# Performance work log

Hardware: AMD Instinct MI355X
Metric: run time of the kernel (lower is better)

Reference implementation:

```python
import jax, jax.numpy as jnp
import numpy as np

NUM_CLASS = 50000
HIDDEN = 512


def setup_inputs() -> dict:
    key = jax.random.key(0)
    ks = jax.random.split(key, 16)
    H, V = HIDDEN, NUM_CLASS
    return {
        # forward args
        "inputX": jax.random.randint(ks[0], (1,), 0, V),
        "hourX": jax.random.randint(ks[1], (1,), 0, 24),
        "weekdayX": jax.random.randint(ks[2], (1,), 0, 7),
        "intervalX": jax.random.uniform(ks[3], (1,), dtype=jnp.float32),
        "h": jax.random.normal(ks[4], (1, H), dtype=jnp.float32),
        "h3": jax.random.normal(ks[5], (1, H), dtype=jnp.float32),
        # parameters (torch Linear convention: weight [out, in])
        "emb": jax.random.normal(ks[6], (V, H), dtype=jnp.float32) * 0.02,
        "W_h3": jax.random.normal(ks[7], (H, H), dtype=jnp.float32) * 0.05,
        "b_h3": jax.random.normal(ks[8], (H,), dtype=jnp.float32) * 0.05,
        "W_int": jax.random.normal(ks[9], (H, 1), dtype=jnp.float32) * 0.05,
        "b_int": jax.random.normal(ks[10], (H,), dtype=jnp.float32) * 0.05,
        "W_ctx": jax.random.normal(ks[11], (H * H, H), dtype=jnp.float32) * 0.02,
        "b_ctx": jax.random.normal(ks[12], (H * H,), dtype=jnp.float32) * 0.02,
        "b_ictx": jax.random.normal(ks[13], (H,), dtype=jnp.float32) * 0.05,
        "Wx": jax.random.normal(ks[14], (H, H), dtype=jnp.float32) * 0.05,
        "Bx": jax.random.normal(ks[15], (H,), dtype=jnp.float32) * 0.05,
        "fc_W": jax.random.normal(jax.random.fold_in(key, 100), (V, H), dtype=jnp.float32) * 0.02,
        "fc_b": jax.random.normal(jax.random.fold_in(key, 101), (V,), dtype=jnp.float32) * 0.02,
    }


def reference(inputX, hourX, weekdayX, intervalX, h, h3,
              emb, W_h3, b_h3, W_int, b_int, W_ctx, b_ctx, b_ictx,
              Wx, Bx, fc_W, fc_b):
    H = h.shape[-1]
    sig = jax.nn.sigmoid
    # embedding lookup: [1, H]
    x_emb = emb[inputX]
    # h3 update: F.linear(intervalX, W_int, b_int) + LinearH3(h3)
    # W_int: [H, 1] so the interval linear is intervalX * W_int[:, 0] + b_int
    h3_new = sig(intervalX[:, None] * W_int[:, 0][None, :] + b_int
                 + h3 @ W_h3.T + b_h3)                      # [1, H]
    # hypernetwork: per-step context weight matrix [H, H]
    ctx = sig(h3_new @ W_ctx.T + b_ctx).reshape(H, H)
    # gated recurrent update
    h_new = sig(x_emb @ Wx.T + Bx + h @ ctx.T + b_ictx)      # [1, H]
    logits = h_new @ fc_W.T + fc_b                           # [1, V]
    # original returns (logits, h, h2, h3); h2 is unused/None
    return logits, h_new, h3_new
```

## Files before the change

### kernel.cpp

```cpp
#include <hip/hip_runtime.h>

#define H 512
#define V 50000

typedef float fx4 __attribute__((ext_vector_type(4)));

__device__ __forceinline__ float sigmoidf(float x) {
    return 1.0f / (1.0f + __expf(-x));
}

__device__ __forceinline__ float wave_reduce(float v) {
    #pragma unroll
    for (int m = 32; m >= 1; m >>= 1)
        v += __shfl_xor(v, m, 64);
    return v;
}

__device__ __forceinline__ float dot4(fx4 a, fx4 b) {
    return a.x * b.x + a.y * b.y + a.z * b.z + a.w * b.w;
}

__device__ __forceinline__ fx4 ntload4(const float* p) {
    return __builtin_nontemporal_load((const fx4*)p);
}

__device__ __forceinline__ fx4 ld4(const float* p) {
    return *(const fx4*)p;
}

__global__ __launch_bounds__(128) void kA(
    const float* __restrict__ intervalX, const float* __restrict__ h3,
    const float* __restrict__ W_h3, const float* __restrict__ b_h3,
    const float* __restrict__ W_int, const float* __restrict__ b_int,
    float* __restrict__ out)
{
    const int tid  = threadIdx.x;
    const int wv   = tid >> 6;
    const int lane = tid & 63;
    const int r    = blockIdx.x * 2 + wv;

    const float* Wrow = W_h3 + (size_t)r * H;
    fx4 a0 = ld4(Wrow + lane * 4);
    fx4 a1 = ld4(Wrow + 256 + lane * 4);
    fx4 x0 = ld4(h3 + lane * 4);
    fx4 x1 = ld4(h3 + 256 + lane * 4);
    float p = dot4(a0, x0) + dot4(a1, x1);
    p = wave_reduce(p);

    if (lane == 0) {
        float pre = p + intervalX[0] * W_int[r] + b_int[r] + b_h3[r];
        out[V + H + r] = sigmoidf(pre);
    }
}

__global__ __launch_bounds__(1024) void kB(
    const int* __restrict__ inputX, const float* __restrict__ emb,
    const float* __restrict__ h, const float* __restrict__ W_ctx,
    const float* __restrict__ b_ctx, const float* __restrict__ h3n,
    const float* __restrict__ Wx, const float* __restrict__ Bx,
    const float* __restrict__ b_ictx, float* __restrict__ out)
{
    __shared__ float sh3[H];
    __shared__ float sh[H];
    __shared__ float semb[H];
    __shared__ float sbc[H];
    __shared__ float red[16];

    const int tid = threadIdx.x;
    const int j   = blockIdx.x;
    const size_t base = (size_t)j * H;

    const float* embrow = emb + (size_t)inputX[0] * H;
    if (tid < H) {
        sh3[tid]  = h3n[tid];
        semb[tid] = embrow[tid];
    } else {
        const int t = tid - H;
        sh[t]  = h[t];
        sbc[t] = b_ctx[base + t];
    }
    __syncthreads();

    const int wv   = tid >> 6;
    const int lane = tid & 63;

    const fx4 x0 = ld4(sh3 + lane * 4);
    const fx4 x1 = ld4(sh3 + 256 + lane * 4);

    float acc = 0.0f;

    if (wv == 0) {
        const float* Wxrow = Wx + (size_t)j * H;
        fx4 a0 = ld4(Wxrow + lane * 4);
        fx4 a1 = ld4(Wxrow + 256 + lane * 4);
        float p = dot4(a0, ld4(semb + lane * 4)) + dot4(a1, ld4(semb + 256 + lane * 4));
        p = wave_reduce(p);
        acc += p + Bx[j] + b_ictx[j];
    }

    if ((j & 3) == 0) {
        #pragma unroll 4
        for (int i = 0; i < 32; ++i) {
            const int k = wv * 32 + i;
            const float* Wrow = W_ctx + (base + (size_t)k) * H;
            fx4 a0 = ld4(Wrow + lane * 4);
            fx4 a1 = ld4(Wrow + 256 + lane * 4);
            float p = dot4(a0, x0) + dot4(a1, x1);
            p = wave_reduce(p);
            acc += sh[k] * sigmoidf(p + sbc[k]);
        }
    } else {
        #pragma unroll 4
        for (int i = 0; i < 32; ++i) {
            const int k = wv * 32 + i;
            const float* Wrow = W_ctx + (base + (size_t)k) * H;
            fx4 a0 = ntload4(Wrow + lane * 4);
            fx4 a1 = ntload4(Wrow + 256 + lane * 4);
            float p = dot4(a0, x0) + dot4(a1, x1);
            p = wave_reduce(p);
            acc += sh[k] * sigmoidf(p + sbc[k]);
        }
    }

    if (lane == 0) red[wv] = acc;
    __syncthreads();

    if (tid == 0) {
        float t = 0.0f;
        #pragma unroll
        for (int w = 0; w < 16; ++w) t += red[w];
        out[V + j] = sigmoidf(t);
    }
}

__global__ __launch_bounds__(256) void kC(
    const float* __restrict__ h_new, const float* __restrict__ fc_W,
    const float* __restrict__ fc_b, float* __restrict__ out)
{
    __shared__ float shn[H];
    const int tid = threadIdx.x;
    shn[tid]       = h_new[tid];
    shn[tid + 256] = h_new[tid + 256];
    __syncthreads();

    const int wv   = tid >> 6;
    const int lane = tid & 63;
    const fx4 x0 = ld4(shn + lane * 4);
    const fx4 x1 = ld4(shn + 256 + lane * 4);

    const int rbase = blockIdx.x * 16 + wv * 4;
    #pragma unroll
    for (int r = 0; r < 4; ++r) {
        const int v = rbase + r;
        const float* Wrow = fc_W + (size_t)v * H;
        fx4 a0 = ld4(Wrow + lane * 4);
        fx4 a1 = ld4(Wrow + 256 + lane * 4);
        float p = dot4(a0, x0) + dot4(a1, x1);
        p = wave_reduce(p);
        if (lane == 0) out[v] = p + fc_b[v];
    }
}

extern "C" void kernel_launch(void* const* d_in, const int* in_sizes, int n_in,
                              void* d_out, int out_size, void* d_ws, size_t ws_size,
                              hipStream_t stream) {
    const int*   inputX    = (const int*)d_in[0];
    const float* intervalX = (const float*)d_in[3];
    const float* h         = (const float*)d_in[4];
    const float* h3        = (const float*)d_in[5];
    const float* emb       = (const float*)d_in[6];
    const float* W_h3      = (const float*)d_in[7];
    const float* b_h3      = (const float*)d_in[8];
    const float* W_int     = (const float*)d_in[9];
    const float* b_int     = (const float*)d_in[10];
    const float* W_ctx     = (const float*)d_in[11];
    const float* b_ctx     = (const float*)d_in[12];
    const float* b_ictx    = (const float*)d_in[13];
    const float* Wx        = (const float*)d_in[14];
    const float* Bx        = (const float*)d_in[15];
    const float* fc_W      = (const float*)d_in[16];
    const float* fc_b      = (const float*)d_in[17];

    float* out = (float*)d_out;

    kA<<<256, 128, 0, stream>>>(intervalX, h3, W_h3, b_h3, W_int, b_int, out);
    kB<<<512, 1024, 0, stream>>>(inputX, emb, h, W_ctx, b_ctx, out + V + H,
                                 Wx, Bx, b_ictx, out);
    kC<<<3125, 256, 0, stream>>>(out + V, fc_W, fc_b, out);
}
```

Measured before the change: 108.5 us.

## Fuse three kernels into one persistent kernel with grid barrier

Merges the h3 update, hypernetwork context GEMV and final logits GEMV into a single 512-block kernel. Each block recomputes h3_new redundantly (256 KB of W_h3 reads per block, mostly served from cache), and an atomic counter acts as a grid-wide barrier before the fc_W phase. This removes two kernel launches and the gaps between them. In exchange it adds a memset, redundant compute, and a spin barrier that deadlocks unless all 512 blocks of 1024 threads are co-resident.

```diff
diff --git a/kernel.cpp b/kernel.cpp
--- a/kernel.cpp
+++ b/kernel.cpp
@@ -2,6 +2,8 @@
 
 #define H 512
 #define V 50000
+#define NBLK 512
+#define NTHR 1024
 
 typedef float fx4 __attribute__((ext_vector_type(4)));
 
@@ -28,73 +30,64 @@
     return *(const fx4*)p;
 }
 
-__global__ __launch_bounds__(128) void kA(
-    const float* __restrict__ intervalX, const float* __restrict__ h3,
+__global__ __launch_bounds__(NTHR, 8) void fused(
+    const int* __restrict__ inputX, const float* __restrict__ intervalX,
+    const float* __restrict__ h, const float* __restrict__ h3,
+    const float* __restrict__ emb,
     const float* __restrict__ W_h3, const float* __restrict__ b_h3,
     const float* __restrict__ W_int, const float* __restrict__ b_int,
-    float* __restrict__ out)
+    const float* __restrict__ W_ctx, const float* __restrict__ b_ctx,
+    const float* __restrict__ b_ictx,
+    const float* __restrict__ Wx, const float* __restrict__ Bx,
+    const float* __restrict__ fc_W, const float* __restrict__ fc_b,
+    float* __restrict__ out, int* __restrict__ cnt)
 {
+    __shared__ float sh3[H];
+    __shared__ float sh[H];
+    __shared__ float sbc[H];
+    __shared__ float red[16];
+
     const int tid  = threadIdx.x;
     const int wv   = tid >> 6;
     const int lane = tid & 63;
-    const int r    = blockIdx.x * 2 + wv;
-
-    const float* Wrow = W_h3 + (size_t)r * H;
-    fx4 a0 = ld4(Wrow + lane * 4);
-    fx4 a1 = ld4(Wrow + 256 + lane * 4);
-    fx4 x0 = ld4(h3 + lane * 4);
-    fx4 x1 = ld4(h3 + 256 + lane * 4);
-    float p = dot4(a0, x0) + dot4(a1, x1);
-    p = wave_reduce(p);
-
-    if (lane == 0) {
-        float pre = p + intervalX[0] * W_int[r] + b_int[r] + b_h3[r];
-        out[V + H + r] = sigmoidf(pre);
-    }
-}
-
-__global__ __launch_bounds__(1024) void kB(
-    const int* __restrict__ inputX, const float* __restrict__ emb,
-    const float* __restrict__ h, const float* __restrict__ W_ctx,
-    const float* __restrict__ b_ctx, const float* __restrict__ h3n,
-    const float* __restrict__ Wx, const float* __restrict__ Bx,
-    const float* __restrict__ b_ictx, float* __restrict__ out)
-{
-    __shared__ float sh3[H];
-    __shared__ float sh[H];
-    __shared__ float semb[H];
-    __shared__ float sbc[H];
-    __shared__ float red[16];
-
-    const int tid = threadIdx.x;
-    const int j   = blockIdx.x;
+    const int j    = blockIdx.x;
     const size_t base = (size_t)j * H;
 
-    const float* embrow = emb + (size_t)inputX[0] * H;
-    if (tid < H) {
-        sh3[tid]  = h3n[tid];
-        semb[tid] = embrow[tid];
-    } else {
-        const int t = tid - H;
-        sh[t]  = h[t];
-        sbc[t] = b_ctx[base + t];
+    if (tid < H) sh[tid] = h[tid];
+    else { const int t = tid - H; sbc[t] = b_ctx[base + t]; }
+
+    {
+        const float ivx = intervalX[0];
+        const fx4 x0 = ld4(h3 + lane * 4);
+        const fx4 x1 = ld4(h3 + 256 + lane * 4);
+        #pragma unroll 4
+        for (int i = 0; i < 32; ++i) {
+            const int k = wv * 32 + i;
+            const float* Wrow = W_h3 + (size_t)k * H;
+            fx4 a0 = ld4(Wrow + lane * 4);
+            fx4 a1 = ld4(Wrow + 256 + lane * 4);
+            float p = wave_reduce(dot4(a0, x0) + dot4(a1, x1));
+            if (lane == 0) {
+                float v = sigmoidf(p + ivx * W_int[k] + b_int[k] + b_h3[k]);
+                sh3[k] = v;
+                if (j == 0) out[V + H + k] = v;
+            }
+        }
     }
     __syncthreads();
-
-    const int wv   = tid >> 6;
-    const int lane = tid & 63;
 
     const fx4 x0 = ld4(sh3 + lane * 4);
     const fx4 x1 = ld4(sh3 + 256 + lane * 4);
 
     float acc = 0.0f;
-
     if (wv == 0) {
         const float* Wxrow = Wx + (size_t)j * H;
+        const float* e = emb + (size_t)inputX[0] * H;
         fx4 a0 = ld4(Wxrow + lane * 4);
         fx4 a1 = ld4(Wxrow + 256 + lane * 4);
-        float p = dot4(a0, ld4(semb + lane * 4)) + dot4(a1, ld4(semb + 256 + lane * 4));
-        p = wave_reduce(p);
+        fx4 e0 = ld4(e + lane * 4);
+        fx4 e1 = ld4(e + 256 + lane * 4);
+        float p = wave_reduce(dot4(a0, e0) + dot4(a1, e1));
         acc += p + Bx[j] + b_ictx[j];
     }
 
@@ -105,8 +98,7 @@
             const float* Wrow = W_ctx + (base + (size_t)k) * H;
             fx4 a0 = ld4(Wrow + lane * 4);
             fx4 a1 = ld4(Wrow + 256 + lane * 4);
-            float p = dot4(a0, x0) + dot4(a1, x1);
-            p = wave_reduce(p);
+            float p = wave_reduce(dot4(a0, x0) + dot4(a1, x1));
             acc += sh[k] * sigmoidf(p + sbc[k]);
         }
     } else {
@@ -116,8 +108,7 @@
             const float* Wrow = W_ctx + (base + (size_t)k) * H;
             fx4 a0 = ntload4(Wrow + lane * 4);
             fx4 a1 = ntload4(Wrow + 256 + lane * 4);
-            float p = dot4(a0, x0) + dot4(a1, x1);
-            p = wave_reduce(p);
+            float p = wave_reduce(dot4(a0, x0) + dot4(a1, x1));
             acc += sh[k] * sigmoidf(p + sbc[k]);
         }
     }
@@ -130,34 +121,31 @@
         #pragma unroll
         for (int w = 0; w < 16; ++w) t += red[w];
         out[V + j] = sigmoidf(t);
+        __threadfence();
+        __hip_atomic_fetch_add(cnt, 1, __ATOMIC_RELEASE, __HIP_MEMORY_SCOPE_AGENT);
+        while (__hip_atomic_load(cnt, __ATOMIC_RELAXED, __HIP_MEMORY_SCOPE_AGENT) < NBLK) {
+            __builtin_amdgcn_s_sleep(2);
+        }
     }
-}
+    __syncthreads();
+    __threadfence();
 
-__global__ __launch_bounds__(256) void kC(
-    const float* __restrict__ h_new, const float* __restrict__ fc_W,
-    const float* __restrict__ fc_b, float* __restrict__ out)
-{
-    __shared__ float shn[H];
-    const int tid = threadIdx.x;
-    shn[tid]       = h_new[tid];
-    shn[tid + 256] = h_new[tid + 256];
+    if (tid < H) sh3[tid] = out[V + tid];
     __syncthreads();
 
-    const int wv   = tid >> 6;
-    const int lane = tid & 63;
-    const fx4 x0 = ld4(shn + lane * 4);
-    const fx4 x1 = ld4(shn + 256 + lane * 4);
+    const fx4 y0 = ld4(sh3 + lane * 4);
+    const fx4 y1 = ld4(sh3 + 256 + lane * 4);
 
-    const int rbase = blockIdx.x * 16 + wv * 4;
-    #pragma unroll
-    for (int r = 0; r < 4; ++r) {
-        const int v = rbase + r;
-        const float* Wrow = fc_W + (size_t)v * H;
-        fx4 a0 = ld4(Wrow + lane * 4);
-        fx4 a1 = ld4(Wrow + 256 + lane * 4);
-        float p = dot4(a0, x0) + dot4(a1, x1);
-        p = wave_reduce(p);
-        if (lane == 0) out[v] = p + fc_b[v];
+    const int rbeg = j * 98;
+    for (int t = wv; t < 98; t += 16) {
+        const int v = rbeg + t;
+        if (v < V) {
+            const float* Wrow = fc_W + (size_t)v * H;
+            fx4 a0 = ld4(Wrow + lane * 4);
+            fx4 a1 = ld4(Wrow + 256 + lane * 4);
+            float p = wave_reduce(dot4(a0, y0) + dot4(a1, y1));
+            if (lane == 0) out[v] = p + fc_b[v];
+        }
     }
 }
 
@@ -182,9 +170,12 @@
     const float* fc_b      = (const float*)d_in[17];
 
     float* out = (float*)d_out;
+    int*   cnt = (int*)d_ws;
 
-    kA<<<256, 128, 0, stream>>>(intervalX, h3, W_h3, b_h3, W_int, b_int, out);
-    kB<<<512, 1024, 0, stream>>>(inputX, emb, h, W_ctx, b_ctx, out + V + H,
-                                 Wx, Bx, b_ictx, out);
-    kC<<<3125, 256, 0, stream>>>(out + V, fc_W, fc_b, out);
+    hipMemsetAsync(d_ws, 0, 64, stream);
+
+    fused<<<NBLK, NTHR, 0, stream>>>(inputX, intervalX, h, h3, emb,
+                                     W_h3, b_h3, W_int, b_int,
+                                     W_ctx, b_ctx, b_ictx, Wx, Bx,
+                                     fc_W, fc_b, out, cnt);
 }
```

New measurement: 305.6 us. 182% more time.
